# Performance work log

Measured on AMD Instinct MI355X. Metric: run time of the kernel, lower is better.

The kernel has to match this reference:

```python
import jax, jax.numpy as jnp
import numpy as np

B, C, D = 16384, 10000, 256
COEF = 1.0
CLAMP_MIN = 1e-12
CLAMP_MAX = 1.0e12


def setup_inputs() -> dict:
    key = jax.random.key(0)
    k1, k2, k3, k4 = jax.random.split(key, 4)
    embeddings = jax.random.normal(k1, (B, D), dtype=jnp.float32)
    outputs = jax.random.normal(k2, (B, C), dtype=jnp.float32)
    target = jax.random.randint(k3, (B,), 0, C, dtype=jnp.int64)
    centers = jax.random.normal(k4, (C, D), dtype=jnp.float32)
    return {"embeddings": embeddings, "outputs": outputs, "target": target, "centers": centers}


def reference(embeddings, outputs, target, centers):
    # Center loss: per-row squared distance to the center of the target class.
    # Equivalent to distmat[i, target[i]] without building the per-row Python loop.
    # distmat = ||e||^2 + ||c||^2 - 2 e @ c^T ; we only need the gathered column.
    e_sq = jnp.sum(embeddings * embeddings, axis=1)                 # [B]
    c_sq = jnp.sum(centers * centers, axis=1)                       # [C]
    cross = jnp.einsum('bd,bd->b', embeddings, centers[target])     # [B] = (e @ c^T)[i, t_i]
    dist = e_sq + c_sq[target] - 2.0 * cross                        # [B]
    dist = jnp.clip(dist, CLAMP_MIN, CLAMP_MAX)
    center_loss = jnp.mean(dist)

    # Cross-entropy (mean over batch) on logits.
    logp = jax.nn.log_softmax(outputs, axis=-1)                     # [B, C]
    nll = -jnp.mean(jnp.take_along_axis(logp, target[:, None], axis=1)[:, 0])

    return center_loss * COEF + nll
```

## Files before the change

### kernel.cpp

```cpp
#include <hip/hip_runtime.h>
#include <math.h>

#define BB 16384
#define CC 10000
#define DD 256
#define COEF 1.0f
#define CLAMP_MIN 1e-12f
#define CLAMP_MAX 1.0e12f

__global__ void zero_out_kernel(float* out) { out[0] = 0.0f; }

__global__ __launch_bounds__(256) void center_ce_kernel(
    const float* __restrict__ embeddings,
    const float* __restrict__ outputs,
    const int*   __restrict__ target,
    const float* __restrict__ centers,
    float*       __restrict__ out)
{
    const int row  = blockIdx.x;
    const int tid  = threadIdx.x;
    const int lane = tid & 63;
    const int wave = tid >> 6;
    const int t    = target[row];

    float ed   = embeddings[(size_t)row * DD + tid];
    float cd   = centers[(size_t)t * DD + tid];
    float diff = ed - cd;
    float dsq  = diff * diff;

    const float4* rowp = (const float4*)(outputs + (size_t)row * CC);
    const int n4 = CC / 4;
    float m = -INFINITY;
    float s = 0.0f;
    for (int idx = tid; idx < n4; idx += 256) {
        float4 v = rowp[idx];
        float mx = fmaxf(fmaxf(v.x, v.y), fmaxf(v.z, v.w));
        if (mx > m) {
            s *= __expf(m - mx);
            m = mx;
        }
        s += __expf(v.x - m) + __expf(v.y - m) + __expf(v.z - m) + __expf(v.w - m);
    }

    for (int off = 32; off > 0; off >>= 1) {
        float om = __shfl_down(m, off, 64);
        float os = __shfl_down(s, off, 64);
        float od = __shfl_down(dsq, off, 64);
        float nm = fmaxf(m, om);
        s = s * __expf(m - nm) + os * __expf(om - nm);
        m = nm;
        dsq += od;
    }

    __shared__ float sm[4], ss[4], sd[4];
    if (lane == 0) { sm[wave] = m; ss[wave] = s; sd[wave] = dsq; }
    __syncthreads();

    if (tid == 0) {
        float M = sm[0], S = ss[0], Dq = sd[0];
        #pragma unroll
        for (int w = 1; w < 4; ++w) {
            float om = sm[w], os = ss[w];
            float nm = fmaxf(M, om);
            S = S * __expf(M - nm) + os * __expf(om - nm);
            M = nm;
            Dq += sd[w];
        }
        float x_t  = outputs[(size_t)row * CC + t];
        float dist = fminf(fmaxf(Dq, CLAMP_MIN), CLAMP_MAX);
        float nll  = -(x_t - M - __logf(S));
        float loss = dist * COEF + nll;
        atomicAdd(out, loss * (1.0f / (float)BB));
    }
}

extern "C" void kernel_launch(void* const* d_in, const int* in_sizes, int n_in,
                              void* d_out, int out_size, void* d_ws, size_t ws_size,
                              hipStream_t stream) {
    const float* embeddings = (const float*)d_in[0];
    const float* outputs    = (const float*)d_in[1];
    const int*   target     = (const int*)  d_in[2];
    const float* centers    = (const float*)d_in[3];
    float* out = (float*)d_out;

    hipLaunchKernelGGL(zero_out_kernel, dim3(1), dim3(1), 0, stream, out);
    hipLaunchKernelGGL(center_ce_kernel, dim3(BB), dim3(256), 0, stream,
                       embeddings, outputs, target, centers, out);
}
```

Baseline: 913.1 us.

## Map one row per wavefront and replace global atomics with a two-pass reduction

Each wavefront now handles a whole row: it reads the embedding and center with float4 loads and runs the online softmax over that row, so a 256-thread block covers four rows. This removes the cross-wave shared-memory merge of softmax state and cuts block count by four. The single global atomicAdd per row is replaced by one partial per block written to workspace, followed by a small reduction kernel, which also removes the zeroing launch and makes the sum deterministic. In exchange each wave streams a longer row on its own, with fewer loads in flight per row.

```diff
diff --git a/kernel.cpp b/kernel.cpp
--- a/kernel.cpp
+++ b/kernel.cpp
@@ -4,41 +4,40 @@
 #define BB 16384
 #define CC 10000
 #define DD 256
+#define N4 (CC / 4)
+#define ROWS_PER_BLOCK 4
+#define NBLK (BB / ROWS_PER_BLOCK)
 #define COEF 1.0f
 #define CLAMP_MIN 1e-12f
 #define CLAMP_MAX 1.0e12f
-
-__global__ void zero_out_kernel(float* out) { out[0] = 0.0f; }
 
 __global__ __launch_bounds__(256) void center_ce_kernel(
     const float* __restrict__ embeddings,
     const float* __restrict__ outputs,
     const int*   __restrict__ target,
     const float* __restrict__ centers,
-    float*       __restrict__ out)
+    float*       __restrict__ partials)
 {
-    const int row  = blockIdx.x;
     const int tid  = threadIdx.x;
     const int lane = tid & 63;
     const int wave = tid >> 6;
+    const int row  = blockIdx.x * ROWS_PER_BLOCK + wave;
     const int t    = target[row];
 
-    float ed   = embeddings[(size_t)row * DD + tid];
-    float cd   = centers[(size_t)t * DD + tid];
-    float diff = ed - cd;
-    float dsq  = diff * diff;
+    const float4* ep = (const float4*)(embeddings + (size_t)row * DD);
+    const float4* cp = (const float4*)(centers    + (size_t)t   * DD);
+    float4 e = ep[lane];
+    float4 c = cp[lane];
+    float dx = e.x - c.x, dy = e.y - c.y, dz = e.z - c.z, dw = e.w - c.w;
+    float dsq = dx * dx + dy * dy + dz * dz + dw * dw;
 
     const float4* rowp = (const float4*)(outputs + (size_t)row * CC);
-    const int n4 = CC / 4;
     float m = -INFINITY;
     float s = 0.0f;
-    for (int idx = tid; idx < n4; idx += 256) {
+    for (int idx = lane; idx < N4; idx += 64) {
         float4 v = rowp[idx];
         float mx = fmaxf(fmaxf(v.x, v.y), fmaxf(v.z, v.w));
-        if (mx > m) {
-            s *= __expf(m - mx);
-            m = mx;
-        }
+        if (mx > m) { s *= __expf(m - mx); m = mx; }
         s += __expf(v.x - m) + __expf(v.y - m) + __expf(v.z - m) + __expf(v.w - m);
     }
 
@@ -52,26 +51,33 @@
         dsq += od;
     }
 
-    __shared__ float sm[4], ss[4], sd[4];
-    if (lane == 0) { sm[wave] = m; ss[wave] = s; sd[wave] = dsq; }
+    __shared__ float sl[ROWS_PER_BLOCK];
+    if (lane == 0) {
+        float x_t  = outputs[(size_t)row * CC + t];
+        float dist = fminf(fmaxf(dsq, CLAMP_MIN), CLAMP_MAX);
+        float nll  = -(x_t - m - __logf(s));
+        sl[wave] = dist * COEF + nll;
+    }
     __syncthreads();
+    if (tid == 0) {
+        float acc = 0.0f;
+        #pragma unroll
+        for (int w = 0; w < ROWS_PER_BLOCK; ++w) acc += sl[w];
+        partials[blockIdx.x] = acc;
+    }
+}
 
-    if (tid == 0) {
-        float M = sm[0], S = ss[0], Dq = sd[0];
-        #pragma unroll
-        for (int w = 1; w < 4; ++w) {
-            float om = sm[w], os = ss[w];
-            float nm = fmaxf(M, om);
-            S = S * __expf(M - nm) + os * __expf(om - nm);
-            M = nm;
-            Dq += sd[w];
-        }
-        float x_t  = outputs[(size_t)row * CC + t];
-        float dist = fminf(fmaxf(Dq, CLAMP_MIN), CLAMP_MAX);
-        float nll  = -(x_t - M - __logf(S));
-        float loss = dist * COEF + nll;
-        atomicAdd(out, loss * (1.0f / (float)BB));
-    }
+__global__ __launch_bounds__(256) void reduce_kernel(
+    const float* __restrict__ partials, float* __restrict__ out)
+{
+    const int tid = threadIdx.x;
+    float acc = 0.0f;
+    for (int i = tid; i < NBLK; i += 256) acc += partials[i];
+    for (int off = 32; off > 0; off >>= 1) acc += __shfl_down(acc, off, 64);
+    __shared__ float sw[4];
+    if ((tid & 63) == 0) sw[tid >> 6] = acc;
+    __syncthreads();
+    if (tid == 0) out[0] = (sw[0] + sw[1] + sw[2] + sw[3]) * (1.0f / (float)BB);
 }
 
 extern "C" void kernel_launch(void* const* d_in, const int* in_sizes, int n_in,
@@ -81,9 +87,11 @@
     const float* outputs    = (const float*)d_in[1];
     const int*   target     = (const int*)  d_in[2];
     const float* centers    = (const float*)d_in[3];
-    float* out = (float*)d_out;
+    float* partials = (float*)d_ws;
+    float* out      = (float*)d_out;
 
-    hipLaunchKernelGGL(zero_out_kernel, dim3(1), dim3(1), 0, stream, out);
-    hipLaunchKernelGGL(center_ce_kernel, dim3(BB), dim3(256), 0, stream,
-                       embeddings, outputs, target, centers, out);
+    hipLaunchKernelGGL(center_ce_kernel, dim3(NBLK), dim3(256), 0, stream,
+                       embeddings, outputs, target, centers, partials);
+    hipLaunchKernelGGL(reduce_kernel, dim3(1), dim3(256), 0, stream,
+                       partials, out);
 }
```

New measurement: 838.0 us. 8.2% less time.
